# Kernel tuning notes

Hardware: AMD Instinct MI355X
Metric: run time of the kernel (lower is better)

Reference implementation:

```python
import jax, jax.numpy as jnp
import numpy as np
import random

NQUBIT = 4
NUM_CIRCUITS = 3
SEED = 1024
C64 = jnp.complex64

SINGLE = ['rx', 'ry', 'rz', 's', 't', 'p', 'u3']
DOUBLE = ['rxx', 'ryy', 'rzz', 'swap', 'cnot', 'cp', 'ch', 'cu', 'ct', 'cz']
PCOUNT = {'rx': 1, 'ry': 1, 'rz': 1, 's': 0, 't': 0, 'p': 1, 'u3': 3,
          'rxx': 1, 'ryy': 1, 'rzz': 1, 'swap': 0, 'cnot': 0, 'cp': 1,
          'ch': 0, 'cu': 3, 'ct': 0, 'cz': 0}


def build_circuits(nqubit=NQUBIT, num_circuits=NUM_CIRCUITS, seed=SEED):
    # Replays the torch module's python `random` stream (random.seed(seed))
    rng = random.Random(seed)
    circuits, off = [], 0
    for _ in range(num_circuits):
        gates = []
        for _blk in range(3):
            for i in range(nqubit):
                g = rng.choice(SINGLE)
                gates.append((g, (i,), off, PCOUNT[g])); off += PCOUNT[g]
            c, t = rng.sample(range(0, nqubit - 1), 2)
            g = rng.choice(DOUBLE)
            gates.append((g, (c, t), off, PCOUNT[g])); off += PCOUNT[g]
        circuits.append(gates)
    return circuits, off


def u3mat(th, ph, lam):
    c = jnp.cos(th * 0.5).astype(C64)
    s = jnp.sin(th * 0.5).astype(C64)
    eip = jnp.exp(1j * ph.astype(C64))
    eil = jnp.exp(1j * lam.astype(C64))
    return jnp.stack([jnp.stack([c, -eil * s]), jnp.stack([eip * s, eip * eil * c])])


def mat1(name, p):
    if name == 's':
        return jnp.array([[1, 0], [0, 1j]], C64)
    if name == 't':
        return jnp.array([[1, 0], [0, np.exp(1j * np.pi / 4)]], C64)
    if name == 'u3':
        return u3mat(p[0], p[1], p[2])
    one = jnp.ones((), C64); zero = jnp.zeros((), C64)
    if name == 'p':
        return jnp.stack([jnp.stack([one, zero]), jnp.stack([zero, jnp.exp(1j * p[0].astype(C64))])])
    h = p[0] * 0.5
    if name == 'rx':
        c = jnp.cos(h).astype(C64); s = (-1j * jnp.sin(h)).astype(C64)
        return jnp.stack([jnp.stack([c, s]), jnp.stack([s, c])])
    if name == 'ry':
        c = jnp.cos(h).astype(C64); s = jnp.sin(h).astype(C64)
        return jnp.stack([jnp.stack([c, -s]), jnp.stack([s, c])])
    if name == 'rz':
        e = jnp.exp(-1j * h.astype(C64))
        return jnp.stack([jnp.stack([e, zero]), jnp.stack([zero, jnp.conj(e)])])
    raise ValueError(name)


def mat2(name, p):
    if name == 'swap':
        return jnp.array([[1, 0, 0, 0], [0, 0, 1, 0], [0, 1, 0, 0], [0, 0, 0, 1]], C64)
    if name == 'cnot':
        return jnp.array([[1, 0, 0, 0], [0, 1, 0, 0], [0, 0, 0, 1], [0, 0, 1, 0]], C64)
    if name == 'cz':
        return jnp.diag(jnp.array([1, 1, 1, -1], C64))
    if name == 'ct':
        return jnp.diag(jnp.array([1, 1, 1, np.exp(1j * np.pi / 4)], C64))
    if name == 'ch':
        m = np.eye(4, dtype=np.complex64); r = 1.0 / np.sqrt(2.0)
        m[2:, 2:] = [[r, r], [r, -r]]
        return jnp.asarray(m)
    if name == 'cp':
        one = jnp.ones((), C64)
        return jnp.diag(jnp.stack([one, one, one, jnp.exp(1j * p[0].astype(C64))]))
    if name == 'cu':
        return jnp.zeros((4, 4), C64).at[:2, :2].set(jnp.eye(2, dtype=C64)).at[2:, 2:].set(u3mat(p[0], p[1], p[2]))
    h = p[0] * 0.5
    if name == 'rzz':
        e = jnp.exp(-1j * h.astype(C64)); ec = jnp.conj(e)
        return jnp.diag(jnp.stack([e, ec, ec, e]))
    if name == 'rxx':
        c = jnp.cos(h).astype(C64); s = (-1j * jnp.sin(h)).astype(C64)
        XX = jnp.array([[0, 0, 0, 1], [0, 0, 1, 0], [0, 1, 0, 0], [1, 0, 0, 0]], C64)
        return c * jnp.eye(4, dtype=C64) + s * XX
    if name == 'ryy':
        c = jnp.cos(h).astype(C64); s = (1j * jnp.sin(h)).astype(C64)
        YY = jnp.array([[0, 0, 0, 1], [0, 0, -1, 0], [0, -1, 0, 0], [1, 0, 0, 0]], C64)
        return c * jnp.eye(4, dtype=C64) + s * YY
    raise ValueError(name)


def apply1(state, U, q):
    # state: (N, 2,2,2,2); contract qubit-q axis with U
    state = jnp.moveaxis(state, 1 + q, -1)
    state = state @ U.T
    return jnp.moveaxis(state, -1, 1 + q)


def apply2(state, U, q0, q1):
    state = jnp.moveaxis(state, (1 + q0, 1 + q1), (-2, -1))
    sh = state.shape
    state = (state.reshape(sh[:-2] + (4,)) @ U.T).reshape(sh)
    return jnp.moveaxis(state, (-2, -1), (1 + q0, 1 + q1))


def zsigns(nqubit):
    idx = np.arange(2 ** nqubit)
    return np.stack([1.0 - 2.0 * ((idx >> (nqubit - 1 - q)) & 1) for q in range(nqubit)]).astype(np.float32)


def run_circuit(angles, params, gates, nqubit):
    N = angles.shape[0]
    h = angles * 0.5
    # rx(angle)|0> = [cos(a/2), -i sin(a/2)] per qubit -> product state (encode layer)
    v = jnp.stack([jnp.cos(h), -1j * jnp.sin(h)], axis=-1).astype(C64)  # (N, nq, 2)
    state = jnp.ones((N,), C64)
    for i in range(nqubit):
        state = state[..., None] * v[:, i].reshape((N,) + (1,) * i + (2,))
    for (name, qs, off, cnt) in gates:
        p = params[off:off + cnt]
        if len(qs) == 1:
            state = apply1(state, mat1(name, p), qs[0])
        else:
            state = apply2(state, mat2(name, p), qs[0], qs[1])
    probs = (state.real ** 2 + state.imag ** 2).reshape(N, -1)
    return probs @ jnp.asarray(zsigns(nqubit)).T  # (N, nqubit) Pauli-Z expectations


def _forward(x, params):
    B, C, H, W = x.shape
    circuits, _ = build_circuits()
    x_unf = jnp.moveaxis(x.reshape(B, C, H // 2, 2, W), 3, 4)  # torch unfold(2, 2, 2)
    xr = x_unf.reshape(-1, NQUBIT)
    exps = [run_circuit(xr, params, g, NQUBIT) for g in circuits]
    return jnp.stack(exps, axis=1).reshape(B, NUM_CIRCUITS, W, W)


def setup_inputs():
    key = jax.random.key(0)
    k1, k2 = jax.random.split(key)
    x = jax.random.normal(k1, (512, 1, 64, 64), jnp.float32)
    _, nparams = build_circuits()
    params = jax.random.uniform(k2, (nparams,), jnp.float32, -np.pi, np.pi)
    return {"x": x, "params": params}


def reference(x, params):
    return _forward(x, params)
```

## Files before the change

kernel.cpp:

```cpp
#include <hip/hip_runtime.h>
#include <stdint.h>


namespace {

typedef _Float16 half8 __attribute__((ext_vector_type(8)));
typedef float float4v __attribute__((ext_vector_type(4)));

struct GateList {
  int ty[45];
  int q0[45];
  int q1[45];
  int off[45];
};

struct PyRandom {
  uint32_t mt[624];
  int mti;
  void init_genrand(uint32_t s) {
    mt[0] = s;
    for (int i = 1; i < 624; ++i)
      mt[i] = 1812433253u * (mt[i - 1] ^ (mt[i - 1] >> 30)) + (uint32_t)i;
    mti = 624;
  }
  void init_by_array(const uint32_t* key, int klen) {
    init_genrand(19650218u);
    int i = 1, j = 0;
    int k = 624 > klen ? 624 : klen;
    for (; k; --k) {
      mt[i] = (mt[i] ^ ((mt[i - 1] ^ (mt[i - 1] >> 30)) * 1664525u)) + key[j] + (uint32_t)j;
      ++i; ++j;
      if (i >= 624) { mt[0] = mt[623]; i = 1; }
      if (j >= klen) j = 0;
    }
    for (k = 623; k; --k) {
      mt[i] = (mt[i] ^ ((mt[i - 1] ^ (mt[i - 1] >> 30)) * 1566083941u)) - (uint32_t)i;
      ++i;
      if (i >= 624) { mt[0] = mt[623]; i = 1; }
    }
    mt[0] = 0x80000000u;
    mti = 624;
  }
  uint32_t genrand() {
    if (mti >= 624) {
      const uint32_t mag[2] = {0u, 0x9908b0dfu};
      int kk; uint32_t y;
      for (kk = 0; kk < 227; ++kk) {
        y = (mt[kk] & 0x80000000u) | (mt[kk + 1] & 0x7fffffffu);
        mt[kk] = mt[kk + 397] ^ (y >> 1) ^ mag[y & 1];
      }
      for (; kk < 623; ++kk) {
        y = (mt[kk] & 0x80000000u) | (mt[kk + 1] & 0x7fffffffu);
        mt[kk] = mt[kk - 227] ^ (y >> 1) ^ mag[y & 1];
      }
      y = (mt[623] & 0x80000000u) | (mt[0] & 0x7fffffffu);
      mt[623] = mt[396] ^ (y >> 1) ^ mag[y & 1];
      mti = 0;
    }
    uint32_t y = mt[mti++];
    y ^= y >> 11;
    y ^= (y << 7) & 0x9d2c5680u;
    y ^= (y << 15) & 0xefc60000u;
    y ^= y >> 18;
    return y;
  }
  uint32_t getrandbits(int k) { return genrand() >> (32 - k); }
  uint32_t randbelow(uint32_t n) {
    int k = 32 - __builtin_clz(n);
    uint32_t r = getrandbits(k);
    while (r >= n) r = getrandbits(k);
    return r;
  }
};

void build_gatelist(GateList& gl) {
  PyRandom rng;
  uint32_t key = 1024u;
  rng.init_by_array(&key, 1);
  static const int PC_S[7]  = {1, 1, 1, 0, 0, 1, 3};
  static const int PC_D[10] = {1, 1, 1, 0, 0, 1, 0, 3, 0, 0};
  int off = 0, idx = 0;
  for (int circ = 0; circ < 3; ++circ) {
    for (int blk = 0; blk < 3; ++blk) {
      for (int i = 0; i < 4; ++i) {
        int g = (int)rng.randbelow(7);
        gl.ty[idx] = g; gl.q0[idx] = i; gl.q1[idx] = 0; gl.off[idx] = off;
        off += PC_S[g]; ++idx;
      }
      int pool[3] = {0, 1, 2};
      int j0 = (int)rng.randbelow(3); int c = pool[j0]; pool[j0] = pool[2];
      int j1 = (int)rng.randbelow(2); int t = pool[j1];
      int g = (int)rng.randbelow(10);
      gl.ty[idx] = 10 + g; gl.q0[idx] = c; gl.q1[idx] = t; gl.off[idx] = off;
      off += PC_D[g]; ++idx;
    }
  }
}

__device__ inline float2 cmul(float2 a, float2 b) {
  return make_float2(a.x * b.x - a.y * b.y, a.x * b.y + a.y * b.x);
}
__device__ inline float2 cadd(float2 a, float2 b) {
  return make_float2(a.x + b.x, a.y + b.y);
}
__device__ inline float2 shflx(float2 v, int m) {
  return make_float2(__shfl_xor(v.x, m), __shfl_xor(v.y, m));
}

__global__ __launch_bounds__(768) void build_T(
    const float* __restrict__ params, _Float16* __restrict__ Tws, GateList gl) {
  __shared__ float2 ldsU[768];
  __shared__ float  ldsA[3072];

  const int tid = threadIdx.x;

  ((uint64_t*)Tws)[tid] = 0ull;

  {
    const int circ = tid >> 8;
    const int col  = (tid >> 4) & 15;
    const int k    = tid & 15;

    float2 s = make_float2(k == col ? 1.f : 0.f, 0.f);

    for (int g = 0; g < 15; ++g) {
      int gi = circ * 15 + g;
      int ty = gl.ty[gi];
      int o  = gl.off[gi];
      if (ty < 7) {
        float2 G00 = make_float2(1, 0), G01 = make_float2(0, 0),
               G10 = make_float2(0, 0), G11 = make_float2(1, 0);
        if (ty == 0) {
          float c, sn; __sincosf(params[o] * 0.5f, &sn, &c);
          G00 = make_float2(c, 0); G01 = make_float2(0, -sn);
          G10 = make_float2(0, -sn); G11 = make_float2(c, 0);
        } else if (ty == 1) {
          float c, sn; __sincosf(params[o] * 0.5f, &sn, &c);
          G00 = make_float2(c, 0); G01 = make_float2(-sn, 0);
          G10 = make_float2(sn, 0); G11 = make_float2(c, 0);
        } else if (ty == 2) {
          float c, sn; __sincosf(params[o] * 0.5f, &sn, &c);
          G00 = make_float2(c, -sn); G11 = make_float2(c, sn);
        } else if (ty == 3) {
          G11 = make_float2(0, 1);
        } else if (ty == 4) {
          G11 = make_float2(0.7071067811865476f, 0.7071067811865476f);
        } else if (ty == 5) {
          float cp, sp; __sincosf(params[o], &sp, &cp);
          G11 = make_float2(cp, sp);
        } else {
          float th = params[o], phv = params[o + 1], lm = params[o + 2];
          float c, sn; __sincosf(th * 0.5f, &sn, &c);
          float cp, sp; __sincosf(phv, &sp, &cp);
          float cl, sl; __sincosf(lm, &sl, &cl);
          G00 = make_float2(c, 0);
          G01 = make_float2(-cl * sn, -sl * sn);
          G10 = make_float2(cp * sn, sp * sn);
          G11 = make_float2((cp * cl - sp * sl) * c, (cp * sl + sp * cl) * c);
        }
        int m = 1 << (3 - gl.q0[gi]);
        bool hib = (k & m) != 0;
        float2 p = shflx(s, m);
        float2 A = hib ? G11 : G00;
        float2 B = hib ? G10 : G01;
        s = cadd(cmul(A, s), cmul(B, p));
      } else {
        float2 G[4][4];
#pragma unroll
        for (int r2 = 0; r2 < 4; ++r2)
#pragma unroll
          for (int c2 = 0; c2 < 4; ++c2) G[r2][c2] = make_float2(0, 0);
        if (ty == 10) {
          float c, sn; __sincosf(params[o] * 0.5f, &sn, &c);
          G[0][0] = G[1][1] = G[2][2] = G[3][3] = make_float2(c, 0);
          G[0][3] = G[1][2] = G[2][1] = G[3][0] = make_float2(0, -sn);
        } else if (ty == 11) {
          float c, sn; __sincosf(params[o] * 0.5f, &sn, &c);
          G[0][0] = G[1][1] = G[2][2] = G[3][3] = make_float2(c, 0);
          G[0][3] = G[3][0] = make_float2(0, sn);
          G[1][2] = G[2][1] = make_float2(0, -sn);
        } else if (ty == 12) {
          float c, sn; __sincosf(params[o] * 0.5f, &sn, &c);
          G[0][0] = G[3][3] = make_float2(c, -sn);
          G[1][1] = G[2][2] = make_float2(c, sn);
        } else if (ty == 13) {
          G[0][0] = make_float2(1, 0); G[1][2] = make_float2(1, 0);
          G[2][1] = make_float2(1, 0); G[3][3] = make_float2(1, 0);
        } else if (ty == 14) {
          G[0][0] = G[1][1] = make_float2(1, 0);
          G[2][3] = G[3][2] = make_float2(1, 0);
        } else if (ty == 15) {
          G[0][0] = G[1][1] = G[2][2] = make_float2(1, 0);
          float cp, sp; __sincosf(params[o], &sp, &cp);
          G[3][3] = make_float2(cp, sp);
        } else if (ty == 16) {
          G[0][0] = G[1][1] = make_float2(1, 0);
          float rv = 0.7071067811865476f;
          G[2][2] = make_float2(rv, 0); G[2][3] = make_float2(rv, 0);
          G[3][2] = make_float2(rv, 0); G[3][3] = make_float2(-rv, 0);
        } else if (ty == 17) {
          G[0][0] = G[1][1] = make_float2(1, 0);
          float th = params[o], phv = params[o + 1], lm = params[o + 2];
          float c, sn; __sincosf(th * 0.5f, &sn, &c);
          float cp, sp; __sincosf(phv, &sp, &cp);
          float cl, sl; __sincosf(lm, &sl, &cl);
          G[2][2] = make_float2(c, 0);
          G[2][3] = make_float2(-cl * sn, -sl * sn);
          G[3][2] = make_float2(cp * sn, sp * sn);
          G[3][3] = make_float2((cp * cl - sp * sl) * c, (cp * sl + sp * cl) * c);
        } else if (ty == 18) {
          G[0][0] = G[1][1] = G[2][2] = make_float2(1, 0);
          G[3][3] = make_float2(0.7071067811865476f, 0.7071067811865476f);
        } else {
          G[0][0] = G[1][1] = G[2][2] = make_float2(1, 0);
          G[3][3] = make_float2(-1, 0);
        }
        int m0 = 1 << (3 - gl.q0[gi]);
        int m1 = 1 << (3 - gl.q1[gi]);
        bool b0 = (k & m0) != 0;
        bool b1 = (k & m1) != 0;
        float2 p0 = s;
        float2 p1 = shflx(s, m1);
        float2 p2 = shflx(s, m0);
        float2 p3 = shflx(s, m0 ^ m1);
        float2 acc = make_float2(0, 0);
#pragma unroll
        for (int jj = 0; jj < 4; ++jj) {
          float2 r0 = b1 ? G[1][1 ^ jj] : G[0][0 ^ jj];
          float2 r1 = b1 ? G[3][3 ^ jj] : G[2][2 ^ jj];
          float2 coef = b0 ? r1 : r0;
          float2 pj = (jj == 0) ? p0 : (jj == 1) ? p1 : (jj == 2) ? p2 : p3;
          acc = cadd(acc, cmul(coef, pj));
        }
        s = acc;
      }
    }

    int pc = __popc(col) & 3;
    float2 ph = make_float2(1, 0);
    if (pc == 1) ph = make_float2(0, -1);
    else if (pc == 2) ph = make_float2(-1, 0);
    else if (pc == 3) ph = make_float2(0, 1);
    float2 v = cmul(s, ph);

    ldsU[(circ * 16 + k) * 16 + col] = v;
  }
  __syncthreads();

  {
    const int circ = tid >> 8;
    const int k    = (tid >> 4) & 15;
    const int l    = tid & 15;
    float a0 = 0.f, a1 = 0.f, a2 = 0.f, a3 = 0.f;
    for (int i = 0; i < 16; ++i) {
      float2 uk = ldsU[(circ * 16 + i) * 16 + k];
      float2 ul = ldsU[(circ * 16 + i) * 16 + l];
      float t = uk.x * ul.x + uk.y * ul.y;
      a0 += (i & 8) ? -t : t;
      a1 += (i & 4) ? -t : t;
      a2 += (i & 2) ? -t : t;
      a3 += (i & 1) ? -t : t;
    }
    ldsA[((circ * 4 + 0) * 16 + k) * 16 + l] = a0;
    ldsA[((circ * 4 + 1) * 16 + k) * 16 + l] = a1;
    ldsA[((circ * 4 + 2) * 16 + k) * 16 + l] = a2;
    ldsA[((circ * 4 + 3) * 16 + k) * 16 + l] = a3;
  }
  __syncthreads();

  for (int idx = tid; idx < 972; idx += 768) {
    int cq = idx / 81;
    int j  = idx - cq * 81;
    int j0 = j / 27, j1 = (j / 9) % 3, j2 = (j % 9) / 3, j3 = j % 3;
    int jarr[4] = {j0, j1, j2, j3};
    float acc = 0.f;
    for (int sel = 0; sel < 16; ++sel) {
      int kk = 0, ll = 0;
      float sg = 1.f;
#pragma unroll
      for (int q = 0; q < 4; ++q) {
        int t = (sel >> (3 - q)) & 1;
        kk |= t << (3 - q);
        int lb = (jarr[q] == 2) ? (1 - t) : t;
        ll |= lb << (3 - q);
        if (jarr[q] == 1 && t) sg = -sg;
      }
      acc += sg * ldsA[(cq * 16 + kk) * 16 + ll];
    }
    float T = acc * 0.0625f;
    _Float16 th = (_Float16)T;
    _Float16 tl = (_Float16)(T - (float)th);
    int mf = j >> 5, kkc = j & 31;
    int L = ((kkc >> 3) << 4) | cq;
    int jj = kkc & 7;
    Tws[((mf * 2 + 0) * 64 + L) * 8 + jj] = th;
    Tws[((mf * 2 + 1) * 64 + L) * 8 + jj] = tl;
  }
}

__global__ __launch_bounds__(256, 3) void qconv_main(
    const float* __restrict__ x, const _Float16* __restrict__ T,
    float* __restrict__ out) {
  __shared__ _Float16 lds[256 * 104];
  const int tid  = threadIdx.x;
  const int wid  = tid >> 6;
  const int lane = tid & 63;
  const int quad = lane >> 4;
  const int n16  = lane & 15;
  const int r = blockIdx.x * 256 + tid;

  const half8* Tv = (const half8*)T;
  half8 afh[3], afl[3];
#pragma unroll
  for (int mf = 0; mf < 3; ++mf) {
    afh[mf] = Tv[(mf * 2 + 0) * 64 + lane];
    afl[mf] = Tv[(mf * 2 + 1) * 64 + lane];
  }

  const int b  = r >> 10;
  const int h2 = (r >> 5) & 31;
  const int j  = r & 31;
  const float* xb = x + b * 4096 + h2 * 128 + j * 2;
  float2 lo = *(const float2*)(xb);
  float2 hi = *(const float2*)(xb + 64);
  float c0, s0, c1, s1, c2, s2, c3, s3;
  __sincosf(lo.x, &s0, &c0);
  __sincosf(hi.x, &s1, &c1);
  __sincosf(lo.y, &s2, &c2);
  __sincosf(hi.y, &s3, &c3);
  float f0[3] = {1.f, c0, s0}, f1[3] = {1.f, c1, s1};
  float f2[3] = {1.f, c2, s2}, f3[3] = {1.f, c3, s3};
  float g01e[11], g23[9];
#pragma unroll
  for (int a = 0; a < 9; ++a) g01e[a] = f0[a / 3] * f1[a % 3];
  g01e[9] = 0.f; g01e[10] = 0.f;
#pragma unroll
  for (int bq = 0; bq < 9; ++bq) g23[bq] = f2[bq / 3] * f3[bq % 3];

#pragma unroll
  for (int w = 0; w < 12; ++w) {
    __align__(16) _Float16 h8[8];
#pragma unroll
    for (int e = 0; e < 8; ++e) {
      const int jg = w * 8 + e;
      h8[e] = (_Float16)(g01e[jg / 9] * g23[jg % 9]);
    }
    *(half8*)&lds[tid * 104 + w * 8] = *(const half8*)h8;
  }
  __syncthreads();

  half8 bf[4][3];
#pragma unroll
  for (int t = 0; t < 4; ++t) {
    const int row = wid * 64 + t * 16 + n16;
#pragma unroll
    for (int mf = 0; mf < 3; ++mf)
      bf[t][mf] = *(const half8*)&lds[row * 104 + mf * 32 + quad * 8];
  }
  float4v acc[4];
#pragma unroll
  for (int t = 0; t < 4; ++t) acc[t] = (float4v){0.f, 0.f, 0.f, 0.f};
#pragma unroll
  for (int mf = 0; mf < 3; ++mf) {
#pragma unroll
    for (int t = 0; t < 4; ++t)
      acc[t] = __builtin_amdgcn_mfma_f32_16x16x32_f16(afl[mf], bf[t][mf], acc[t], 0, 0, 0);
#pragma unroll
    for (int t = 0; t < 4; ++t)
      acc[t] = __builtin_amdgcn_mfma_f32_16x16x32_f16(afh[mf], bf[t][mf], acc[t], 0, 0, 0);
  }

  if (quad < 3) {
#pragma unroll
    for (int t = 0; t < 4; ++t) {
      int rowg = blockIdx.x * 256 + wid * 64 + t * 16 + n16;
      *(float4*)(out + (size_t)rowg * 12 + quad * 4) =
          make_float4(acc[t][0], acc[t][1], acc[t][2], acc[t][3]);
    }
  }
}

}

extern "C" void kernel_launch(void* const* d_in, const int* in_sizes, int n_in,
                              void* d_out, int out_size, void* d_ws, size_t ws_size,
                              hipStream_t stream) {
  const float* x      = (const float*)d_in[0];
  const float* params = (const float*)d_in[1];
  float* out = (float*)d_out;
  _Float16* Tws = (_Float16*)d_ws;

  GateList gl;
  build_gatelist(gl);

  hipLaunchKernelGGL(build_T, dim3(1), dim3(768), 0, stream, params, Tws, gl);

  int nrows = in_sizes[0] / 4;
  int grid  = nrows / 256;
  hipLaunchKernelGGL(qconv_main, dim3(grid), dim3(256), 0, stream,
                     x, Tws, out);
}
```

Before: 82.92 us.

## Factor qubit-0 features out of LDS feature tile and rebuild B operand in registers

The per-row 81-term feature vector is no longer fully materialised in LDS. Only the 27-term product of qubits 1-3 plus the three qubit-0 factors are stored, and each MFMA B fragment is rebuilt by scaling that slice by the qubit-0 factor in half precision. The T table layout in build_T is reindexed to match the new mf-major ordering. This cuts LDS footprint and stores enough to raise the launch-bounds occupancy hint to 4, and moves the T loads after the barrier. Output stores become nontemporal. The extra fp16 multiply slightly changes rounding and adds VALU work before the MFMAs.

```diff
diff --git a/kernel.cpp b/kernel.cpp
--- a/kernel.cpp
+++ b/kernel.cpp
@@ -5,6 +5,7 @@
 namespace {
 
 typedef _Float16 half8 __attribute__((ext_vector_type(8)));
+typedef _Float16 half4 __attribute__((ext_vector_type(4)));
 typedef float float4v __attribute__((ext_vector_type(4)));
 
 struct GateList {
@@ -252,6 +253,7 @@
     const int k    = (tid >> 4) & 15;
     const int l    = tid & 15;
     float a0 = 0.f, a1 = 0.f, a2 = 0.f, a3 = 0.f;
+#pragma unroll
     for (int i = 0; i < 16; ++i) {
       float2 uk = ldsU[(circ * 16 + i) * 16 + k];
       float2 ul = ldsU[(circ * 16 + i) * 16 + l];
@@ -268,11 +270,12 @@
   }
   __syncthreads();
 
-  for (int idx = tid; idx < 972; idx += 768) {
-    int cq = idx / 81;
-    int j  = idx - cq * 81;
-    int j0 = j / 27, j1 = (j / 9) % 3, j2 = (j % 9) / 3, j3 = j % 3;
-    int jarr[4] = {j0, j1, j2, j3};
+  for (int idx = tid; idx < 1152; idx += 768) {
+    int cq = idx / 96;
+    int K  = idx - cq * 96;
+    int mf = K >> 5, r = K & 31;
+    if (r >= 27) continue;
+    int jarr[4] = {mf, r / 9, (r / 3) % 3, r % 3};
     float acc = 0.f;
     for (int sel = 0; sel < 16; ++sel) {
       int kk = 0, ll = 0;
@@ -290,32 +293,23 @@
     float T = acc * 0.0625f;
     _Float16 th = (_Float16)T;
     _Float16 tl = (_Float16)(T - (float)th);
-    int mf = j >> 5, kkc = j & 31;
-    int L = ((kkc >> 3) << 4) | cq;
-    int jj = kkc & 7;
+    int L  = ((r >> 3) << 4) | cq;
+    int jj = r & 7;
     Tws[((mf * 2 + 0) * 64 + L) * 8 + jj] = th;
     Tws[((mf * 2 + 1) * 64 + L) * 8 + jj] = tl;
   }
 }
 
-__global__ __launch_bounds__(256, 3) void qconv_main(
+__global__ __launch_bounds__(256, 4) void qconv_main(
     const float* __restrict__ x, const _Float16* __restrict__ T,
     float* __restrict__ out) {
-  __shared__ _Float16 lds[256 * 104];
+  __shared__ _Float16 lds[256 * 40];
   const int tid  = threadIdx.x;
   const int wid  = tid >> 6;
   const int lane = tid & 63;
   const int quad = lane >> 4;
   const int n16  = lane & 15;
   const int r = blockIdx.x * 256 + tid;
-
-  const half8* Tv = (const half8*)T;
-  half8 afh[3], afl[3];
-#pragma unroll
-  for (int mf = 0; mf < 3; ++mf) {
-    afh[mf] = Tv[(mf * 2 + 0) * 64 + lane];
-    afl[mf] = Tv[(mf * 2 + 1) * 64 + lane];
-  }
 
   const int b  = r >> 10;
   const int h2 = (r >> 5) & 31;
@@ -328,54 +322,73 @@
   __sincosf(hi.x, &s1, &c1);
   __sincosf(lo.y, &s2, &c2);
   __sincosf(hi.y, &s3, &c3);
-  float f0[3] = {1.f, c0, s0}, f1[3] = {1.f, c1, s1};
-  float f2[3] = {1.f, c2, s2}, f3[3] = {1.f, c3, s3};
-  float g01e[11], g23[9];
-#pragma unroll
-  for (int a = 0; a < 9; ++a) g01e[a] = f0[a / 3] * f1[a % 3];
-  g01e[9] = 0.f; g01e[10] = 0.f;
-#pragma unroll
-  for (int bq = 0; bq < 9; ++bq) g23[bq] = f2[bq / 3] * f3[bq % 3];
-
-#pragma unroll
-  for (int w = 0; w < 12; ++w) {
-    __align__(16) _Float16 h8[8];
-#pragma unroll
-    for (int e = 0; e < 8; ++e) {
-      const int jg = w * 8 + e;
-      h8[e] = (_Float16)(g01e[jg / 9] * g23[jg % 9]);
-    }
-    *(half8*)&lds[tid * 104 + w * 8] = *(const half8*)h8;
+
+  float f1a[3] = {1.f, c1, s1};
+  float f23[9];
+  {
+    float f2a[3] = {1.f, c2, s2}, f3a[3] = {1.f, c3, s3};
+#pragma unroll
+    for (int a = 0; a < 9; ++a) f23[a] = f2a[a / 3] * f3a[a % 3];
+  }
+  __align__(16) _Float16 gh[32];
+#pragma unroll
+  for (int r1 = 0; r1 < 3; ++r1)
+#pragma unroll
+    for (int b9 = 0; b9 < 9; ++b9)
+      gh[r1 * 9 + b9] = (_Float16)(f1a[r1] * f23[b9]);
+#pragma unroll
+  for (int e = 27; e < 32; ++e) gh[e] = (_Float16)0.f;
+
+  {
+    half8* dst = (half8*)&lds[tid * 40];
+    dst[0] = *(const half8*)&gh[0];
+    dst[1] = *(const half8*)&gh[8];
+    dst[2] = *(const half8*)&gh[16];
+    dst[3] = *(const half8*)&gh[24];
+    half4 f0h = {(_Float16)1.f, (_Float16)c0, (_Float16)s0, (_Float16)0.f};
+    *(half4*)&lds[tid * 40 + 32] = f0h;
   }
   __syncthreads();
 
-  half8 bf[4][3];
+  const half8* Tv = (const half8*)T;
+  half8 afh[3], afl[3];
+#pragma unroll
+  for (int mf = 0; mf < 3; ++mf) {
+    afh[mf] = Tv[(mf * 2 + 0) * 64 + lane];
+    afl[mf] = Tv[(mf * 2 + 1) * 64 + lane];
+  }
+
+  half8 slice[4];
+  half4 f0v[4];
 #pragma unroll
   for (int t = 0; t < 4; ++t) {
     const int row = wid * 64 + t * 16 + n16;
-#pragma unroll
-    for (int mf = 0; mf < 3; ++mf)
-      bf[t][mf] = *(const half8*)&lds[row * 104 + mf * 32 + quad * 8];
-  }
+    slice[t] = *(const half8*)&lds[row * 40 + quad * 8];
+    f0v[t]   = *(const half4*)&lds[row * 40 + 32];
+  }
+
   float4v acc[4];
 #pragma unroll
   for (int t = 0; t < 4; ++t) acc[t] = (float4v){0.f, 0.f, 0.f, 0.f};
 #pragma unroll
   for (int mf = 0; mf < 3; ++mf) {
 #pragma unroll
-    for (int t = 0; t < 4; ++t)
-      acc[t] = __builtin_amdgcn_mfma_f32_16x16x32_f16(afl[mf], bf[t][mf], acc[t], 0, 0, 0);
-#pragma unroll
-    for (int t = 0; t < 4; ++t)
-      acc[t] = __builtin_amdgcn_mfma_f32_16x16x32_f16(afh[mf], bf[t][mf], acc[t], 0, 0, 0);
+    for (int t = 0; t < 4; ++t) {
+      _Float16 f0s = f0v[t][mf];
+      half8 bf;
+#pragma unroll
+      for (int e = 0; e < 8; ++e) bf[e] = slice[t][e] * f0s;
+      acc[t] = __builtin_amdgcn_mfma_f32_16x16x32_f16(afl[mf], bf, acc[t], 0, 0, 0);
+      acc[t] = __builtin_amdgcn_mfma_f32_16x16x32_f16(afh[mf], bf, acc[t], 0, 0, 0);
+    }
   }
 
   if (quad < 3) {
 #pragma unroll
     for (int t = 0; t < 4; ++t) {
       int rowg = blockIdx.x * 256 + wid * 64 + t * 16 + n16;
-      *(float4*)(out + (size_t)rowg * 12 + quad * 4) =
-          make_float4(acc[t][0], acc[t][1], acc[t][2], acc[t][3]);
+      float4v ev = acc[t];
+      __builtin_nontemporal_store(ev, (float4v*)(out + (size_t)rowg * 12 + quad * 4));
     }
   }
 }
```

After: 81.41 us. No clear change (-1.8%).
